# Kernel optimization log

Measured on AMD Instinct MI355X. Metric: run time of the kernel, lower is better.

Reference implementation:

```python
import jax, jax.numpy as jnp
import numpy as np

N, E, F, H, L, G, C = 100000, 3200000, 128, 64, 3, 128, 2
BN_EPS = 1e-5


def setup_inputs() -> dict:
    key = jax.random.key(0)
    ks = jax.random.split(key, 16)
    def nrm(k, s, sc=0.05):
        return jax.random.normal(k, s, dtype=jnp.float32) * sc
    return {
        "x": jax.random.normal(ks[0], (N, F), dtype=jnp.float32),
        "lin0_W": nrm(ks[1], (F, H)), "lin0_b": nrm(ks[2], (H,)),
        "eps": jnp.zeros((L,), jnp.float32),                      # GINConv eps per layer
        "W1": nrm(ks[3], (L, H, 2 * H)), "b1": nrm(ks[4], (L, 2 * H)),
        "g1": jnp.ones((L, 2 * H), jnp.float32), "be1": jnp.zeros((L, 2 * H), jnp.float32),
        "W2": nrm(ks[5], (L, 2 * H, H)), "b2": nrm(ks[6], (L, H)),
        "gbn": jnp.ones((L - 1, H), jnp.float32), "bbn": jnp.zeros((L - 1, H), jnp.float32),
        "gate_W": nrm(ks[7], (H, 1)), "gate_b": nrm(ks[8], (1,)),
        "pred_W": nrm(ks[9], (H, H)), "pred_b": nrm(ks[10], (H,)),
        "cls_W": nrm(ks[11], (H, C)), "cls_b": nrm(ks[12], (C,)),
        "edge_index": jax.random.randint(ks[13], (2, E), 0, N),
        "batch": jnp.sort(jax.random.randint(ks[14], (N,), 0, G)),
        "num_graphs": G,
    }


def batchnorm(h, gamma, beta):
    # training-mode BN over node axis, biased variance (torch semantics)
    mu = h.mean(axis=0)
    var = h.var(axis=0)
    return gamma * (h - mu) * jax.lax.rsqrt(var + BN_EPS) + beta


def gin_conv(h, src, dst, eps, W1, b1, g1, be1, W2, b2):
    # message = relu(x_j), aggr='add' at destination
    agg = jax.ops.segment_sum(jax.nn.relu(h[src]), dst, num_segments=h.shape[0])
    z = (1.0 + eps) * h + agg
    z = batchnorm(z @ W1 + b1, g1, be1)          # [N, 2H]
    return jax.nn.relu(z) @ W2 + b2              # [N, H]


def reference(x, lin0_W, lin0_b, eps, W1, b1, g1, be1, W2, b2,
              gbn, bbn, gate_W, gate_b, pred_W, pred_b, cls_W, cls_b,
              edge_index, batch, num_graphs):
    src, dst = edge_index[0], edge_index[1]
    h = x @ lin0_W + lin0_b                      # lin0
    h = gin_conv(h, src, dst, eps[0], W1[0], b1[0], g1[0], be1[0], W2[0], b2[0])
    for i in range(1, L):                        # convs + external BN (not after conv1)
        h = gin_conv(h, src, dst, eps[i], W1[i], b1[i], g1[i], be1[i], W2[i], b2[i])
        h = batchnorm(h, gbn[i - 1], bbn[i - 1])
    # attentional aggregation: segment softmax over gate, weighted sum per graph
    gate = h @ gate_W + gate_b                   # [N, 1]
    gmax = jax.ops.segment_max(gate, batch, num_segments=num_graphs)
    w = jnp.exp(gate - gmax[batch])
    wsum = jax.ops.segment_sum(w, batch, num_segments=num_graphs)
    alpha = w / wsum[batch]                      # [N, 1]
    pooled = jax.ops.segment_sum(alpha * h, batch, num_segments=num_graphs)  # [G, H]
    z = jax.nn.relu(pooled @ pred_W + pred_b)
    return z @ cls_W + cls_b                     # [G, C]
```

## Files before the change

### kernel.cpp

```cpp
#include <hip/hip_runtime.h>
#include <hip/hip_bf16.h>

#define NN 100000
#define EE 3200000
#define HH 64
#define H2 128
#define LL 3
#define GG 128
#define BN_EPSF 1e-5f

#define NBUK 782
#define NBLKC 800
#define CHUNK 4000
#define DMAX 5120

static __device__ __forceinline__ float waveReduceSum64(float v){
  #pragma unroll
  for (int off = 32; off > 0; off >>= 1) v += __shfl_xor(v, off, 64);
  return v;
}

__global__ __launch_bounds__(256) void kA(const int* __restrict__ dst, int* __restrict__ cntmat){
  __shared__ int hist[NBUK];
  int t = threadIdx.x, blk = blockIdx.x;
  for (int j = t; j < NBUK; j += 256) hist[j] = 0;
  __syncthreads();
  int base = blk * CHUNK;
  for (int i = t; i < CHUNK; i += 256){
    int d = dst[base + i];
    atomicAdd(&hist[d >> 7], 1);
  }
  __syncthreads();
  for (int j = t; j < NBUK; j += 256) cntmat[j * NBLKC + blk] = hist[j];
}

__global__ __launch_bounds__(1024) void kB1(int* __restrict__ cntmat, int* __restrict__ btotal){
  __shared__ int s[1024];
  int t = threadIdx.x, j = blockIdx.x;
  int v = (t < NBLKC) ? cntmat[j * NBLKC + t] : 0;
  s[t] = v; __syncthreads();
  for (int off = 1; off < 1024; off <<= 1){
    int x = (t >= off) ? s[t - off] : 0; __syncthreads();
    s[t] += x; __syncthreads();
  }
  if (t < NBLKC) cntmat[j * NBLKC + t] = s[t] - v;
  if (t == 1023) btotal[j] = s[t];
}

__global__ __launch_bounds__(1024) void kB2(const int* __restrict__ btotal,
                                            int* __restrict__ bucket_start,
                                            int* __restrict__ row_start){
  __shared__ int s[1024];
  int t = threadIdx.x;
  int v = (t < NBUK) ? btotal[t] : 0;
  s[t] = v; __syncthreads();
  for (int off = 1; off < 1024; off <<= 1){
    int x = (t >= off) ? s[t - off] : 0; __syncthreads();
    s[t] += x; __syncthreads();
  }
  if (t < NBUK) bucket_start[t] = s[t] - v;
  if (t == 0){ bucket_start[NBUK] = EE; row_start[NN] = EE; }
}

__global__ __launch_bounds__(256) void kC(const int* __restrict__ src, const int* __restrict__ dst,
                                          const int* __restrict__ cntmat,
                                          const int* __restrict__ bucket_start,
                                          int2* __restrict__ epart){
  __shared__ int off_s[NBUK];
  __shared__ int cur_s[NBUK];
  int t = threadIdx.x, blk = blockIdx.x;
  for (int j = t; j < NBUK; j += 256){
    off_s[j] = bucket_start[j] + cntmat[j * NBLKC + blk];
    cur_s[j] = 0;
  }
  __syncthreads();
  int base = blk * CHUNK;
  for (int i = t; i < CHUNK; i += 256){
    int s0 = src[base + i];
    int d0 = dst[base + i];
    int j = d0 >> 7;
    int loc = atomicAdd(&cur_s[j], 1);
    epart[off_s[j] + loc] = make_int2(s0, d0);
  }
}

__global__ __launch_bounds__(256) void kD(const int2* __restrict__ epart,
                                          const int* __restrict__ bucket_start,
                                          int* __restrict__ row_start, int* __restrict__ elist){
  __shared__ int src_s[DMAX];
  __shared__ short dloc_s[DMAX];
  __shared__ int elist_s[DMAX];
  __shared__ int cnts[128];
  __shared__ int scan_s[128];
  int t = threadIdx.x, b = blockIdx.x;
  int bb = bucket_start[b], be = bucket_start[b + 1];
  int cnt = be - bb;
  int node_base = b << 7;
  if (t < 128) cnts[t] = 0;
  __syncthreads();
  for (int i = t; i < cnt; i += 256){
    int2 p = epart[bb + i];
    src_s[i] = p.x;
    int dl = p.y - node_base;
    dloc_s[i] = (short)dl;
    atomicAdd(&cnts[dl], 1);
  }
  __syncthreads();
  if (t < 128) scan_s[t] = cnts[t];
  __syncthreads();
  for (int off = 1; off < 128; off <<= 1){
    int x = 0;
    if (t < 128 && t >= off) x = scan_s[t - off];
    __syncthreads();
    if (t < 128) scan_s[t] += x;
    __syncthreads();
  }
  if (t < 128){
    int e = scan_s[t] - cnts[t];
    int node = node_base + t;
    if (node < NN) row_start[node] = bb + e;
    cnts[t] = e;
  }
  __syncthreads();
  for (int i = t; i < cnt; i += 256){
    int pos = atomicAdd(&cnts[(int)dloc_s[i]], 1);
    elist_s[pos] = src_s[i];
  }
  __syncthreads();
  for (int i = t; i < cnt; i += 256) elist[bb + i] = elist_s[i];
}

__global__ __launch_bounds__(256, 4) void k_gemm1(const float* __restrict__ h,
                                                  const int* __restrict__ row_start,
                                                  const int* __restrict__ elist,
                                                  const float* __restrict__ W1,
                                                  const float* __restrict__ b1,
                                                  const float* __restrict__ epsArr,
                                                  int layer,
                                                  float* __restrict__ y1,
                                                  double* __restrict__ stats){
  alignas(16) __shared__ float Zs[64 * 64];
  __shared__ float redS[128];
  __shared__ float redQ[128];
  int t = threadIdx.x;
  int R0 = blockIdx.x * 64;
  float epsv = 1.0f + epsArr[layer];
  {
    int r  = t >> 2;
    int kq = (t & 3) * 16;
    int R  = R0 + r;
    float zacc[16];
    if (R < NN){
      const float4* hr = (const float4*)&h[(long long)R * 64 + kq];
      #pragma unroll
      for (int i = 0; i < 4; ++i){
        float4 v = hr[i];
        zacc[4*i+0] = epsv * v.x; zacc[4*i+1] = epsv * v.y;
        zacc[4*i+2] = epsv * v.z; zacc[4*i+3] = epsv * v.w;
      }
      int beg = row_start[R], end = row_start[R + 1];
      int j = beg;
      for (; j + 1 < end; j += 2){
        int s0 = elist[j], s1 = elist[j + 1];
        const float4* p0 = (const float4*)&h[(long long)s0 * 64 + kq];
        const float4* p1 = (const float4*)&h[(long long)s1 * 64 + kq];
        float4 a0 = p0[0], a1 = p0[1], a2 = p0[2], a3 = p0[3];
        float4 b0 = p1[0], b1v = p1[1], b2 = p1[2], b3 = p1[3];
        zacc[0]  += fmaxf(a0.x,0.f) + fmaxf(b0.x,0.f);
        zacc[1]  += fmaxf(a0.y,0.f) + fmaxf(b0.y,0.f);
        zacc[2]  += fmaxf(a0.z,0.f) + fmaxf(b0.z,0.f);
        zacc[3]  += fmaxf(a0.w,0.f) + fmaxf(b0.w,0.f);
        zacc[4]  += fmaxf(a1.x,0.f) + fmaxf(b1v.x,0.f);
        zacc[5]  += fmaxf(a1.y,0.f) + fmaxf(b1v.y,0.f);
        zacc[6]  += fmaxf(a1.z,0.f) + fmaxf(b1v.z,0.f);
        zacc[7]  += fmaxf(a1.w,0.f) + fmaxf(b1v.w,0.f);
        zacc[8]  += fmaxf(a2.x,0.f) + fmaxf(b2.x,0.f);
        zacc[9]  += fmaxf(a2.y,0.f) + fmaxf(b2.y,0.f);
        zacc[10] += fmaxf(a2.z,0.f) + fmaxf(b2.z,0.f);
        zacc[11] += fmaxf(a2.w,0.f) + fmaxf(b2.w,0.f);
        zacc[12] += fmaxf(a3.x,0.f) + fmaxf(b3.x,0.f);
        zacc[13] += fmaxf(a3.y,0.f) + fmaxf(b3.y,0.f);
        zacc[14] += fmaxf(a3.z,0.f) + fmaxf(b3.z,0.f);
        zacc[15] += fmaxf(a3.w,0.f) + fmaxf(b3.w,0.f);
      }
      if (j < end){
        int s0 = elist[j];
        const float4* p0 = (const float4*)&h[(long long)s0 * 64 + kq];
        #pragma unroll
        for (int i = 0; i < 4; ++i){
          float4 v = p0[i];
          zacc[4*i+0] += fmaxf(v.x, 0.f); zacc[4*i+1] += fmaxf(v.y, 0.f);
          zacc[4*i+2] += fmaxf(v.z, 0.f); zacc[4*i+3] += fmaxf(v.w, 0.f);
        }
      }
    } else {
      #pragma unroll
      for (int i = 0; i < 16; ++i) zacc[i] = 0.f;
    }
    #pragma unroll
    for (int i = 0; i < 16; ++i) Zs[r * 64 + kq + i] = zacc[i];
  }
  __syncthreads();
  int c = t & 31, rg = t >> 5;
  int r0 = rg * 8;
  float a0[8], a1[8], a2[8], a3[8];
  #pragma unroll
  for (int r = 0; r < 8; ++r){ a0[r]=0.f; a1[r]=0.f; a2[r]=0.f; a3[r]=0.f; }
  for (int k4 = 0; k4 < 16; ++k4){
    float w0[4], w1[4], w2[4], w3[4];
    #pragma unroll
    for (int kk = 0; kk < 4; ++kk){
      int k = k4 * 4 + kk;
      w0[kk] = W1[k*128 + c];
      w1[kk] = W1[k*128 + c + 32];
      w2[kk] = W1[k*128 + c + 64];
      w3[kk] = W1[k*128 + c + 96];
    }
    #pragma unroll
    for (int r = 0; r < 8; ++r){
      float4 zv = *(const float4*)&Zs[(r0 + r) * 64 + k4 * 4];
      a0[r] += zv.x*w0[0] + zv.y*w0[1] + zv.z*w0[2] + zv.w*w0[3];
      a1[r] += zv.x*w1[0] + zv.y*w1[1] + zv.z*w1[2] + zv.w*w1[3];
      a2[r] += zv.x*w2[0] + zv.y*w2[1] + zv.z*w2[2] + zv.w*w2[3];
      a3[r] += zv.x*w3[0] + zv.y*w3[1] + zv.z*w3[2] + zv.w*w3[3];
    }
  }
  float b0 = b1[c], bb1 = b1[c+32], bb2 = b1[c+64], bb3 = b1[c+96];
  float s0=0,s1=0,s2=0,s3=0,q0=0,q1=0,q2=0,q3=0;
  #pragma unroll
  for (int r = 0; r < 8; ++r){
    int R = R0 + r0 + r;
    if (R < NN){
      float y0 = a0[r] + b0, yA = a1[r] + bb1, yB = a2[r] + bb2, yC = a3[r] + bb3;
      long long base = (long long)R * 128;
      y1[base + c]      = y0;
      y1[base + c + 32] = yA;
      y1[base + c + 64] = yB;
      y1[base + c + 96] = yC;
      s0 += y0; q0 += y0*y0; s1 += yA; q1 += yA*yA;
      s2 += yB; q2 += yB*yB; s3 += yC; q3 += yC*yC;
    }
  }
  __syncthreads();
  if (t < 128){ redS[t] = 0.f; redQ[t] = 0.f; }
  __syncthreads();
  atomicAdd(&redS[c],      s0); atomicAdd(&redQ[c],      q0);
  atomicAdd(&redS[c + 32], s1); atomicAdd(&redQ[c + 32], q1);
  atomicAdd(&redS[c + 64], s2); atomicAdd(&redQ[c + 64], q2);
  atomicAdd(&redS[c + 96], s3); atomicAdd(&redQ[c + 96], q3);
  __syncthreads();
  if (t < 128){
    atomicAdd(&stats[t],       (double)redS[t]);
    atomicAdd(&stats[128 + t], (double)redQ[t]);
  }
}

__global__ __launch_bounds__(256, 4) void k_gemm_k128(const float* __restrict__ in,
                                                      const float* __restrict__ W,
                                                      const float* __restrict__ b,
                                                      const float* __restrict__ bnp,
                                                      float* __restrict__ out,
                                                      double* __restrict__ stats,
                                                      int mode){
  alignas(16) __shared__ float As[64 * 128];
  __shared__ float redS[64];
  __shared__ float redQ[64];
  int t = threadIdx.x;
  int R0 = blockIdx.x * 64;
  {
    const float4* in4 = (const float4*)in;
    float4* As4 = (float4*)As;
    #pragma unroll
    for (int i = 0; i < 8; ++i){
      int idx = t + i * 256;
      int r = idx >> 5;
      int R = R0 + r;
      float4 v = make_float4(0.f, 0.f, 0.f, 0.f);
      if (R < NN){
        v = in4[(long long)R * 32 + (idx & 31)];
        if (mode & 1){
          int k = (idx & 31) * 4;
          v.x = fmaxf(v.x * bnp[k]   + bnp[128 + k],     0.f);
          v.y = fmaxf(v.y * bnp[k+1] + bnp[128 + k + 1], 0.f);
          v.z = fmaxf(v.z * bnp[k+2] + bnp[128 + k + 2], 0.f);
          v.w = fmaxf(v.w * bnp[k+3] + bnp[128 + k + 3], 0.f);
        }
      }
      As4[idx] = v;
    }
  }
  __syncthreads();
  int c = t & 31, rg = t >> 5;
  int r0 = rg * 8;
  float a0[8], a1[8];
  #pragma unroll
  for (int r = 0; r < 8; ++r){ a0[r]=0.f; a1[r]=0.f; }
  for (int k4 = 0; k4 < 32; ++k4){
    float w0[4], w1[4];
    #pragma unroll
    for (int kk = 0; kk < 4; ++kk){
      int k = k4 * 4 + kk;
      w0[kk] = W[k*64 + c];
      w1[kk] = W[k*64 + c + 32];
    }
    #pragma unroll
    for (int r = 0; r < 8; ++r){
      float4 a = *(const float4*)&As[(r0 + r) * 128 + k4 * 4];
      a0[r] += a.x*w0[0] + a.y*w0[1] + a.z*w0[2] + a.w*w0[3];
      a1[r] += a.x*w1[0] + a.y*w1[1] + a.z*w1[2] + a.w*w1[3];
    }
  }
  float b0 = b[c], bA = b[c + 32];
  float s0=0,s1=0,q0=0,q1=0;
  #pragma unroll
  for (int r = 0; r < 8; ++r){
    int R = R0 + r0 + r;
    if (R < NN){
      float y0 = a0[r] + b0, yA = a1[r] + bA;
      long long base = (long long)R * 64;
      out[base + c] = y0;
      out[base + c + 32] = yA;
      s0 += y0; q0 += y0*y0; s1 += yA; q1 += yA*yA;
    }
  }
  if (mode & 2){
    __syncthreads();
    if (t < 64){ redS[t] = 0.f; redQ[t] = 0.f; }
    __syncthreads();
    atomicAdd(&redS[c], s0);      atomicAdd(&redQ[c], q0);
    atomicAdd(&redS[c + 32], s1); atomicAdd(&redQ[c + 32], q1);
    __syncthreads();
    if (t < 64){
      atomicAdd(&stats[t],      (double)redS[t]);
      atomicAdd(&stats[64 + t], (double)redQ[t]);
    }
  }
}

__global__ void k_bnfin(const double* __restrict__ stats, const float* __restrict__ gamma,
                        const float* __restrict__ beta, float* __restrict__ bnp, int C){
  int t = threadIdx.x;
  if (t < C){
    double s = stats[t], q = stats[C + t];
    double mu = s / (double)NN;
    double var = q / (double)NN - mu * mu;
    float rstd = rsqrtf((float)var + BN_EPSF);
    float sc = gamma[t] * rstd;
    bnp[t] = sc;
    bnp[C + t] = beta[t] - (float)mu * sc;
  }
}

__global__ __launch_bounds__(256) void k_affine(float* __restrict__ h, const float* __restrict__ bnp){
  int i = blockIdx.x * 256 + threadIdx.x;
  float4* h4 = (float4*)h;
  float4 v = h4[i];
  int base = (i * 4) & 63;
  v.x = v.x * bnp[base + 0] + bnp[64 + base + 0];
  v.y = v.y * bnp[base + 1] + bnp[64 + base + 1];
  v.z = v.z * bnp[base + 2] + bnp[64 + base + 2];
  v.w = v.w * bnp[base + 3] + bnp[64 + base + 3];
  h4[i] = v;
}

__global__ __launch_bounds__(256) void k_gate(const float* __restrict__ h, const float* __restrict__ gateW,
                                              const float* __restrict__ gateB, const int* __restrict__ batch,
                                              float* __restrict__ gate, unsigned* __restrict__ gmaxkey){
  int lane = threadIdx.x & 63;
  int wid = blockIdx.x * 4 + (threadIdx.x >> 6);
  int nwaves = gridDim.x * 4;
  int chunk = (NN + nwaves - 1) / nwaves;
  int n0 = wid * chunk;
  int n1 = n0 + chunk; if (n1 > NN) n1 = NN;
  if (n0 >= NN) return;
  float gw = gateW[lane];
  float gb = gateB[0];
  int gcur = batch[n0];
  float mcur = -3.402823466e+38f;
  for (int n = n0; n < n1; ++n){
    int g = batch[n];
    if (g != gcur){
      if (lane == 0){
        unsigned u = __float_as_uint(mcur);
        u = (u & 0x80000000u) ? ~u : (u | 0x80000000u);
        atomicMax(&gmaxkey[gcur], u);
      }
      gcur = g;
      mcur = -3.402823466e+38f;
    }
    float v = h[(long long)n * 64 + lane] * gw;
    v = waveReduceSum64(v) + gb;
    if (lane == 0) gate[n] = v;
    mcur = fmaxf(mcur, v);
  }
  if (lane == 0){
    unsigned u = __float_as_uint(mcur);
    u = (u & 0x80000000u) ? ~u : (u | 0x80000000u);
    atomicMax(&gmaxkey[gcur], u);
  }
}

__global__ __launch_bounds__(256) void k_pool(const float* __restrict__ h, const float* __restrict__ gate,
                                              const int* __restrict__ batch, const unsigned* __restrict__ gmaxkey,
                                              float* __restrict__ wsum, float* __restrict__ pooled){
  int lane = threadIdx.x & 63;
  int wid = blockIdx.x * 4 + (threadIdx.x >> 6);
  int nwaves = gridDim.x * 4;
  int chunk = (NN + nwaves - 1) / nwaves;
  int n0 = wid * chunk;
  int n1 = n0 + chunk; if (n1 > NN) n1 = NN;
  if (n0 >= NN) return;
  int gcur = batch[n0];
  unsigned u = gmaxkey[gcur];
  unsigned bits = (u & 0x80000000u) ? (u ^ 0x80000000u) : ~u;
  float m = __uint_as_float(bits);
  float acc = 0.f, wl = 0.f;
  for (int n = n0; n < n1; ++n){
    int g = batch[n];
    if (g != gcur){
      atomicAdd(&pooled[gcur * 64 + lane], acc);
      if (lane == 0) atomicAdd(&wsum[gcur], wl);
      gcur = g;
      u = gmaxkey[g];
      bits = (u & 0x80000000u) ? (u ^ 0x80000000u) : ~u;
      m = __uint_as_float(bits);
      acc = 0.f; wl = 0.f;
    }
    float w = expf(gate[n] - m);
    acc += w * h[(long long)n * 64 + lane];
    wl += w;
  }
  atomicAdd(&pooled[gcur * 64 + lane], acc);
  if (lane == 0) atomicAdd(&wsum[gcur], wl);
}

__global__ __launch_bounds__(64) void k_head(const float* __restrict__ pooled, const float* __restrict__ wsum,
                                             const float* __restrict__ predW, const float* __restrict__ predB,
                                             const float* __restrict__ clsW, const float* __restrict__ clsB,
                                             float* __restrict__ out){
  int g = blockIdx.x, lane = threadIdx.x;
  __shared__ float p[64];
  p[lane] = pooled[g * 64 + lane] / wsum[g];
  __syncthreads();
  float acc = predB[lane];
  for (int i = 0; i < 64; ++i) acc += p[i] * predW[i * 64 + lane];
  float z = fmaxf(acc, 0.f);
  float c0 = z * clsW[lane * 2 + 0];
  float c1 = z * clsW[lane * 2 + 1];
  c0 = waveReduceSum64(c0);
  c1 = waveReduceSum64(c1);
  if (lane == 0){
    out[g * 2 + 0] = c0 + clsB[0];
    out[g * 2 + 1] = c1 + clsB[1];
  }
}

extern "C" void kernel_launch(void* const* d_in, const int* in_sizes, int n_in,
                              void* d_out, int out_size, void* d_ws, size_t ws_size,
                              hipStream_t stream){
  const float* x     = (const float*)d_in[0];
  const float* lin0W = (const float*)d_in[1];
  const float* lin0b = (const float*)d_in[2];
  const float* eps   = (const float*)d_in[3];
  const float* W1    = (const float*)d_in[4];
  const float* b1    = (const float*)d_in[5];
  const float* g1    = (const float*)d_in[6];
  const float* be1   = (const float*)d_in[7];
  const float* W2    = (const float*)d_in[8];
  const float* b2    = (const float*)d_in[9];
  const float* gbn   = (const float*)d_in[10];
  const float* bbn   = (const float*)d_in[11];
  const float* gateW = (const float*)d_in[12];
  const float* gateB = (const float*)d_in[13];
  const float* predW = (const float*)d_in[14];
  const float* predB = (const float*)d_in[15];
  const float* clsW  = (const float*)d_in[16];
  const float* clsB  = (const float*)d_in[17];
  const int* eidx    = (const int*)d_in[18];
  const int* batch   = (const int*)d_in[19];
  const int* src = eidx;
  const int* dst = eidx + EE;
  float* out = (float*)d_out;

  char* ws = (char*)d_ws;
  size_t off = 0;
  auto alloc = [&](size_t bytes) -> char* {
    char* p = ws + off;
    off += (bytes + 15) & ~(size_t)15;
    return p;
  };
  float* h       = (float*)alloc((size_t)NN * 64 * 4);
  float* y1      = (float*)alloc((size_t)NN * 128 * 4);
  int* elist     = (int*)alloc((size_t)EE * 4);
  int* row_start = (int*)alloc((size_t)(NN + 1) * 4);
  float* gate    = (float*)alloc((size_t)NN * 4);
  double* stats1 = (double*)alloc(256 * 8);
  double* stats2 = (double*)alloc(128 * 8);
  float* bnp1    = (float*)alloc(256 * 4);
  float* bnp2    = (float*)alloc(128 * 4);
  unsigned* gmaxkey = (unsigned*)alloc(128 * 4);
  float* wsum    = (float*)alloc(128 * 4);
  float* pooled  = (float*)alloc(128 * 64 * 4);

  char* ov = (char*)y1;
  int2* epart       = (int2*)ov;
  int*  cntmat      = (int*)(ov + (size_t)EE * 8);
  int*  btotal      = (int*)(ov + (size_t)EE * 8 + (size_t)NBUK * NBLKC * 4);
  int*  bucket_start= (int*)(ov + (size_t)EE * 8 + (size_t)NBUK * NBLKC * 4 + 3136);

  const int GBLK = (NN + 63) / 64;

  kA <<<NBLKC, 256, 0, stream>>>(dst, cntmat);
  kB1<<<NBUK, 1024, 0, stream>>>(cntmat, btotal);
  kB2<<<1, 1024, 0, stream>>>(btotal, bucket_start, row_start);
  kC <<<NBLKC, 256, 0, stream>>>(src, dst, cntmat, bucket_start, epart);
  kD <<<NBUK, 256, 0, stream>>>(epart, bucket_start, row_start, elist);

  k_gemm_k128<<<GBLK, 256, 0, stream>>>(x, lin0W, lin0b, bnp1, h, stats2, 0);

  for (int l = 0; l < LL; ++l){
    hipMemsetAsync(stats1, 0, 256 * 8, stream);
    k_gemm1<<<GBLK, 256, 0, stream>>>(h, row_start, elist, W1 + (size_t)l * 64 * 128,
                                      b1 + l * 128, eps, l, y1, stats1);
    k_bnfin<<<1, 128, 0, stream>>>(stats1, g1 + l * 128, be1 + l * 128, bnp1, 128);
    if (l > 0) hipMemsetAsync(stats2, 0, 128 * 8, stream);
    int mode = 1 | (l > 0 ? 2 : 0);
    k_gemm_k128<<<GBLK, 256, 0, stream>>>(y1, W2 + (size_t)l * 128 * 64, b2 + l * 64,
                                          bnp1, h, stats2, mode);
    if (l > 0){
      k_bnfin<<<1, 64, 0, stream>>>(stats2, gbn + (l - 1) * 64, bbn + (l - 1) * 64, bnp2, 64);
      k_affine<<<(NN * 64 / 4) / 256, 256, 0, stream>>>(h, bnp2);
    }
  }

  hipMemsetAsync(gmaxkey, 0, 128 * 4, stream);
  hipMemsetAsync(wsum, 0, 128 * 4, stream);
  hipMemsetAsync(pooled, 0, 128 * 64 * 4, stream);
  k_gate<<<1024, 256, 0, stream>>>(h, gateW, gateB, batch, gate, gmaxkey);
  k_pool<<<1024, 256, 0, stream>>>(h, gate, batch, gmaxkey, wsum, pooled);
  k_head<<<128, 64, 0, stream>>>(pooled, wsum, predW, predB, clsW, clsB, out);
}
```

Measured before the change: 1.036 ms.

## Gather pre-ReLU'd bf16 copy of node features in GIN aggregation

Producers of h now also write a bf16 copy with ReLU applied and round-to-nearest-even. The neighbor gather in k_gemm1 reads this copy, halving the bytes per gathered row, and is unrolled four edges deep with no per-element max. This targets the random-gather bandwidth of 3.2M edges per layer, which likely dominates. The cost is an extra 12.8MB write per producer pass and reduced precision in the aggregated messages, which could affect tolerance.

```diff
diff --git a/kernel.cpp b/kernel.cpp
--- a/kernel.cpp
+++ b/kernel.cpp
@@ -18,6 +18,22 @@
   #pragma unroll
   for (int off = 32; off > 0; off >>= 1) v += __shfl_xor(v, off, 64);
   return v;
+}
+
+static __device__ __forceinline__ unsigned bf16rne(float f){
+  unsigned u = __float_as_uint(f);
+  return (u + 0x7FFFu + ((u >> 16) & 1u)) >> 16;
+}
+
+static __device__ __forceinline__ void acc16(float* z, uint4 A, uint4 B){
+  z[0]  += __uint_as_float(A.x << 16); z[1]  += __uint_as_float(A.x & 0xFFFF0000u);
+  z[2]  += __uint_as_float(A.y << 16); z[3]  += __uint_as_float(A.y & 0xFFFF0000u);
+  z[4]  += __uint_as_float(A.z << 16); z[5]  += __uint_as_float(A.z & 0xFFFF0000u);
+  z[6]  += __uint_as_float(A.w << 16); z[7]  += __uint_as_float(A.w & 0xFFFF0000u);
+  z[8]  += __uint_as_float(B.x << 16); z[9]  += __uint_as_float(B.x & 0xFFFF0000u);
+  z[10] += __uint_as_float(B.y << 16); z[11] += __uint_as_float(B.y & 0xFFFF0000u);
+  z[12] += __uint_as_float(B.z << 16); z[13] += __uint_as_float(B.z & 0xFFFF0000u);
+  z[14] += __uint_as_float(B.w << 16); z[15] += __uint_as_float(B.w & 0xFFFF0000u);
 }
 
 __global__ __launch_bounds__(256) void kA(const int* __restrict__ dst, int* __restrict__ cntmat){
@@ -131,6 +147,7 @@
 }
 
 __global__ __launch_bounds__(256, 4) void k_gemm1(const float* __restrict__ h,
+                                                  const unsigned short* __restrict__ hb,
                                                   const int* __restrict__ row_start,
                                                   const int* __restrict__ elist,
                                                   const float* __restrict__ W1,
@@ -160,38 +177,23 @@
       }
       int beg = row_start[R], end = row_start[R + 1];
       int j = beg;
-      for (; j + 1 < end; j += 2){
-        int s0 = elist[j], s1 = elist[j + 1];
-        const float4* p0 = (const float4*)&h[(long long)s0 * 64 + kq];
-        const float4* p1 = (const float4*)&h[(long long)s1 * 64 + kq];
-        float4 a0 = p0[0], a1 = p0[1], a2 = p0[2], a3 = p0[3];
-        float4 b0 = p1[0], b1v = p1[1], b2 = p1[2], b3 = p1[3];
-        zacc[0]  += fmaxf(a0.x,0.f) + fmaxf(b0.x,0.f);
-        zacc[1]  += fmaxf(a0.y,0.f) + fmaxf(b0.y,0.f);
-        zacc[2]  += fmaxf(a0.z,0.f) + fmaxf(b0.z,0.f);
-        zacc[3]  += fmaxf(a0.w,0.f) + fmaxf(b0.w,0.f);
-        zacc[4]  += fmaxf(a1.x,0.f) + fmaxf(b1v.x,0.f);
-        zacc[5]  += fmaxf(a1.y,0.f) + fmaxf(b1v.y,0.f);
-        zacc[6]  += fmaxf(a1.z,0.f) + fmaxf(b1v.z,0.f);
-        zacc[7]  += fmaxf(a1.w,0.f) + fmaxf(b1v.w,0.f);
-        zacc[8]  += fmaxf(a2.x,0.f) + fmaxf(b2.x,0.f);
-        zacc[9]  += fmaxf(a2.y,0.f) + fmaxf(b2.y,0.f);
-        zacc[10] += fmaxf(a2.z,0.f) + fmaxf(b2.z,0.f);
-        zacc[11] += fmaxf(a2.w,0.f) + fmaxf(b2.w,0.f);
-        zacc[12] += fmaxf(a3.x,0.f) + fmaxf(b3.x,0.f);
-        zacc[13] += fmaxf(a3.y,0.f) + fmaxf(b3.y,0.f);
-        zacc[14] += fmaxf(a3.z,0.f) + fmaxf(b3.z,0.f);
-        zacc[15] += fmaxf(a3.w,0.f) + fmaxf(b3.w,0.f);
+      for (; j + 3 < end; j += 4){
+        int s0 = elist[j], s1 = elist[j+1], s2 = elist[j+2], s3 = elist[j+3];
+        const uint4* q0 = (const uint4*)(hb + (size_t)s0 * 64 + kq);
+        const uint4* q1 = (const uint4*)(hb + (size_t)s1 * 64 + kq);
+        const uint4* q2 = (const uint4*)(hb + (size_t)s2 * 64 + kq);
+        const uint4* q3 = (const uint4*)(hb + (size_t)s3 * 64 + kq);
+        uint4 A0 = q0[0], B0 = q0[1];
+        uint4 A1 = q1[0], B1 = q1[1];
+        uint4 A2 = q2[0], B2 = q2[1];
+        uint4 A3 = q3[0], B3 = q3[1];
+        acc16(zacc, A0, B0); acc16(zacc, A1, B1);
+        acc16(zacc, A2, B2); acc16(zacc, A3, B3);
       }
-      if (j < end){
+      for (; j < end; ++j){
         int s0 = elist[j];
-        const float4* p0 = (const float4*)&h[(long long)s0 * 64 + kq];
-        #pragma unroll
-        for (int i = 0; i < 4; ++i){
-          float4 v = p0[i];
-          zacc[4*i+0] += fmaxf(v.x, 0.f); zacc[4*i+1] += fmaxf(v.y, 0.f);
-          zacc[4*i+2] += fmaxf(v.z, 0.f); zacc[4*i+3] += fmaxf(v.w, 0.f);
-        }
+        const uint4* q0 = (const uint4*)(hb + (size_t)s0 * 64 + kq);
+        acc16(zacc, q0[0], q0[1]);
       }
     } else {
       #pragma unroll
@@ -260,6 +262,7 @@
                                                       const float* __restrict__ b,
                                                       const float* __restrict__ bnp,
                                                       float* __restrict__ out,
+                                                      unsigned short* __restrict__ hb,
                                                       double* __restrict__ stats,
                                                       int mode){
   alignas(16) __shared__ float As[64 * 128];
@@ -320,6 +323,8 @@
       long long base = (long long)R * 64;
       out[base + c] = y0;
       out[base + c + 32] = yA;
+      hb[base + c]      = (unsigned short)bf16rne(fmaxf(y0, 0.f));
+      hb[base + c + 32] = (unsigned short)bf16rne(fmaxf(yA, 0.f));
       s0 += y0; q0 += y0*y0; s1 += yA; q1 += yA*yA;
     }
   }
@@ -351,7 +356,8 @@
   }
 }
 
-__global__ __launch_bounds__(256) void k_affine(float* __restrict__ h, const float* __restrict__ bnp){
+__global__ __launch_bounds__(256) void k_affine(float* __restrict__ h, unsigned short* __restrict__ hb,
+                                                const float* __restrict__ bnp){
   int i = blockIdx.x * 256 + threadIdx.x;
   float4* h4 = (float4*)h;
   float4 v = h4[i];
@@ -361,6 +367,10 @@
   v.z = v.z * bnp[base + 2] + bnp[64 + base + 2];
   v.w = v.w * bnp[base + 3] + bnp[64 + base + 3];
   h4[i] = v;
+  unsigned w0 = bf16rne(fmaxf(v.x, 0.f)) | (bf16rne(fmaxf(v.y, 0.f)) << 16);
+  unsigned w1 = bf16rne(fmaxf(v.z, 0.f)) | (bf16rne(fmaxf(v.w, 0.f)) << 16);
+  int row = i >> 4;
+  *(uint2*)(hb + (size_t)row * 64 + base) = make_uint2(w0, w1);
 }
 
 __global__ __launch_bounds__(256) void k_gate(const float* __restrict__ h, const float* __restrict__ gateW,
@@ -492,6 +502,7 @@
   float* h       = (float*)alloc((size_t)NN * 64 * 4);
   float* y1      = (float*)alloc((size_t)NN * 128 * 4);
   int* elist     = (int*)alloc((size_t)EE * 4);
+  unsigned short* hb = (unsigned short*)alloc((size_t)NN * 64 * 2);
   int* row_start = (int*)alloc((size_t)(NN + 1) * 4);
   float* gate    = (float*)alloc((size_t)NN * 4);
   double* stats1 = (double*)alloc(256 * 8);
@@ -516,20 +527,20 @@
   kC <<<NBLKC, 256, 0, stream>>>(src, dst, cntmat, bucket_start, epart);
   kD <<<NBUK, 256, 0, stream>>>(epart, bucket_start, row_start, elist);
 
-  k_gemm_k128<<<GBLK, 256, 0, stream>>>(x, lin0W, lin0b, bnp1, h, stats2, 0);
+  k_gemm_k128<<<GBLK, 256, 0, stream>>>(x, lin0W, lin0b, bnp1, h, hb, stats2, 0);
 
   for (int l = 0; l < LL; ++l){
     hipMemsetAsync(stats1, 0, 256 * 8, stream);
-    k_gemm1<<<GBLK, 256, 0, stream>>>(h, row_start, elist, W1 + (size_t)l * 64 * 128,
+    k_gemm1<<<GBLK, 256, 0, stream>>>(h, hb, row_start, elist, W1 + (size_t)l * 64 * 128,
                                       b1 + l * 128, eps, l, y1, stats1);
     k_bnfin<<<1, 128, 0, stream>>>(stats1, g1 + l * 128, be1 + l * 128, bnp1, 128);
     if (l > 0) hipMemsetAsync(stats2, 0, 128 * 8, stream);
     int mode = 1 | (l > 0 ? 2 : 0);
     k_gemm_k128<<<GBLK, 256, 0, stream>>>(y1, W2 + (size_t)l * 128 * 64, b2 + l * 64,
-                                          bnp1, h, stats2, mode);
+                                          bnp1, h, hb, stats2, mode);
     if (l > 0){
       k_bnfin<<<1, 64, 0, stream>>>(stats2, gbn + (l - 1) * 64, bbn + (l - 1) * 64, bnp2, 64);
-      k_affine<<<(NN * 64 / 4) / 256, 256, 0, stream>>>(h, bnp2);
+      k_affine<<<(NN * 64 / 4) / 256, 256, 0, stream>>>(h, hb, bnp2);
     }
   }
 
```

New measurement: 898.0 us. -13.3%, faster.
